# Kernel optimization log

Measured on AMD Instinct MI355X. Metric: run time of the kernel, lower is better.

Reference implementation:

```python
import jax, jax.numpy as jnp
import numpy as np

B, L = 32, 2048
AA_VOCAB, AA_EMB = 26, 5
C = 256                 # num_channels
S = 8                   # prot_section_size
GO_VOCAB, GO = 30000, 256
K = 15                  # conv kernel size


def setup_inputs() -> dict:
    key = jax.random.key(0)
    ks = jax.random.split(key, 10)
    inp = {
        "input_seq": jax.random.randint(ks[0], (B, L), 0, AA_VOCAB),
        "input_go_term": jax.random.randint(ks[1], (B,), 0, GO_VOCAB),
        "aa_emb": jax.random.normal(ks[2], (AA_VOCAB, AA_EMB), jnp.float32),
        "conv1_w": jax.random.normal(ks[3], (2 * C, AA_EMB, K), jnp.float32) * 0.05,
        "conv1_b": jnp.zeros((2 * C,), jnp.float32),
        "conv2_w": jax.random.normal(ks[4], (C, 2 * C, K), jnp.float32) * 0.02,
        "conv2_b": jnp.zeros((C,), jnp.float32),
        "go_table": jax.random.normal(ks[5], (GO_VOCAB, GO), jnp.float32),
        "attn_w": jax.random.normal(ks[6], (GO, C * S), jnp.float32) * 0.02,
        "attn_b": jnp.zeros((GO,), jnp.float32),
    }
    return inp


def reference(input_seq, input_go_term, aa_emb, conv1_w, conv1_b,
              conv2_w, conv2_b, go_table, attn_w, attn_b):
    # --- ProteinEncoder (dropout = identity at inference) ---
    x = aa_emb[input_seq]                      # [B, L, 5]
    x = jnp.transpose(x, (0, 2, 1))            # [B, 5, L]
    dn = ('NCH', 'OIH', 'NCH')
    x = jax.lax.conv_general_dilated(x, conv1_w, (1,), 'VALID', dimension_numbers=dn)
    x = jax.nn.relu(x + conv1_b[None, :, None])   # [B, 2C, L-14]
    x = jax.lax.conv_general_dilated(x, conv2_w, (1,), 'VALID', dimension_numbers=dn)
    x = jax.nn.relu(x + conv2_b[None, :, None])   # [B, C, P], P = L-28

    # --- section the protein (same row-major view as torch .view) ---
    b, c, P = x.shape
    n = P // S
    rem = P % S
    head = rem // 2
    tail = P - (rem - head)
    enc = x[:, :, head:tail].reshape(b, c * S, n)   # [B, C*S, N]

    # --- Attn('general'): score_i = go . (W @ section_i + bias), softmax over i ---
    go = go_table[input_go_term]                     # [B, G]
    proj = jnp.einsum('bpn,gp->bgn', enc, attn_w) + attn_b[:, None]  # [B, G, N]
    energies = jnp.einsum('bg,bgn->bn', go, proj)    # [B, N]
    attn = jax.nn.softmax(energies, axis=-1)         # [B, N]

    # --- context: [B,1,N] bmm [B,N,C*S] -> [B, C*S] ---
    ctx = jnp.einsum('bn,bpn->bp', attn, enc)
    return ctx
```

## Files before the change

### kernel.cpp

```cpp
#include <hip/hip_runtime.h>

#define B_ 32
#define L_ 2048
#define C1 512
#define C2 256
#define KW 15
#define P1 2034
#define NJ 2016
#define NSEC 252
#define GOD 256

typedef _Float16 f16;
typedef __attribute__((ext_vector_type(4))) _Float16 f16x4;
typedef __attribute__((ext_vector_type(8))) _Float16 f16x8;
typedef __attribute__((ext_vector_type(4))) float f32x4;

#define WS_Y1T   0ull
#define WS_W2R   66650112ull
#define WS_W1R   70582272ull
#define WS_E     70688768ull
#define WS_V     103718912ull
#define WS_EN    103981056ull
#define WS_ATTN  104013312ull

__device__ __forceinline__ void gl16(const f16* g, f16* l) {
    __builtin_amdgcn_global_load_lds((const __attribute__((address_space(1))) char*)(g),
                                     (__attribute__((address_space(3))) char*)(l), 16, 0, 0);
}

__global__ void k_w2r(const float* __restrict__ w2, f16* __restrict__ w2r) {
    const int n = C2 * C1 * KW;
    for (int idx = blockIdx.x * blockDim.x + threadIdx.x; idx < n; idx += gridDim.x * blockDim.x) {
        int o = idx / (C1 * KW);
        int rem = idx - o * (C1 * KW);
        int c = rem / KW;
        int k = rem - c * KW;
        w2r[((size_t)k * C2 + o) * C1 + c] = (f16)w2[idx];
    }
}

__global__ void k_w1r(const float* __restrict__ w1, f16* __restrict__ w1r) {
    const int n = C1 * 104;
    for (int idx = blockIdx.x * blockDim.x + threadIdx.x; idx < n; idx += gridDim.x * blockDim.x) {
        int o = idx / 104;
        int col = idx - o * 104;
        int e = col >> 4, k = col & 15;
        float val = (e < 5 && k < 15) ? w1[o * 75 + e * 15 + k] : 0.f;
        w1r[idx] = (f16)val;
    }
}

__global__ __launch_bounds__(256) void k_conv1(const int* __restrict__ seq,
                                               const float* __restrict__ aa_emb,
                                               const f16* __restrict__ w1r,
                                               const float* __restrict__ b1,
                                               f16* __restrict__ y1t) {
    __shared__ f16 Aw[256 * 104];
    __shared__ f16 Bx[64 * 104];
    __shared__ float xs[5][80];
    const int b = blockIdx.z, o0 = blockIdx.y * 256, pos0 = blockIdx.x * 64;
    const int tid = threadIdx.x;
    const int wave = tid >> 6, lane = tid & 63;
    const int lm = lane & 15, lh = lane >> 4;

#pragma unroll
    for (int r = 0; r < 13; ++r) {
        int q = r * 4096 + wave * 1024 + lane * 16;
        gl16(w1r + o0 * 104 + (q >> 1), Aw + (q >> 1));
    }
    if (tid < 79) {
        int l = pos0 + tid;
        if (l < L_) {
            int a = seq[b * L_ + l];
#pragma unroll
            for (int e = 0; e < 5; ++e) xs[e][tid] = aa_emb[a * 5 + e];
        } else {
#pragma unroll
            for (int e = 0; e < 5; ++e) xs[e][tid] = 0.f;
        }
    }
    __syncthreads();
    for (int idx = tid; idx < 64 * 104; idx += 256) {
        int j = idx / 104, col = idx - j * 104;
        int e = col >> 4, k = col & 15;
        Bx[idx] = (e < 5 && k < 15) ? (f16)xs[e][j + k] : (f16)0.f;
    }
    __syncthreads();

    f32x4 acc[4][4];
#pragma unroll
    for (int mf = 0; mf < 4; ++mf)
#pragma unroll
        for (int nf = 0; nf < 4; ++nf) acc[mf][nf] = (f32x4){0.f, 0.f, 0.f, 0.f};

    const char* Ab = (const char*)Aw + (wave * 64 + lm) * 208 + lh * 16;
    const char* Bb = (const char*)Bx + lm * 208 + lh * 16;
#pragma unroll
    for (int ks = 0; ks < 3; ++ks) {
        f16x8 av[4], bv[4];
#pragma unroll
        for (int mf = 0; mf < 4; ++mf) av[mf] = *(const f16x8*)(Ab + mf * 16 * 208 + ks * 64);
#pragma unroll
        for (int nf = 0; nf < 4; ++nf) bv[nf] = *(const f16x8*)(Bb + nf * 16 * 208 + ks * 64);
#pragma unroll
        for (int mf = 0; mf < 4; ++mf)
#pragma unroll
            for (int nf = 0; nf < 4; ++nf)
                acc[mf][nf] = __builtin_amdgcn_mfma_f32_16x16x32_f16(av[mf], bv[nf], acc[mf][nf], 0, 0, 0);
    }

#pragma unroll
    for (int nf = 0; nf < 4; ++nf) {
        int pos = pos0 + nf * 16 + lm;
        if (pos >= P1) continue;
#pragma unroll
        for (int mf = 0; mf < 4; ++mf) {
            int ob = wave * 64 + mf * 16 + lh * 4;
            f16x4 st;
#pragma unroll
            for (int r = 0; r < 4; ++r)
                st[r] = (f16)fmaxf(acc[mf][nf][r] + b1[o0 + ob + r], 0.f);
            *(f16x4*)(y1t + ((size_t)b * P1 + pos) * C1 + o0 + ob) = st;
        }
    }
}

__global__ __launch_bounds__(256, 2) void k_conv2(const f16* __restrict__ y1t,
                                                  const f16* __restrict__ w2r,
                                                  const float* __restrict__ b2,
                                                  const float* __restrict__ v,
                                                  f16* __restrict__ E,
                                                  float* __restrict__ energies) {
    __shared__ f16 As[3 * 8192];
    __shared__ f16 Bs[10240];
    const int b = blockIdx.y;
    const int n0 = blockIdx.x << 7;
    const int tid = threadIdx.x;
    const int wave = tid >> 6, lane = tid & 63;
    const int lm = lane & 15, lh = lane >> 4;
    const int wm = wave >> 1, wn = wave & 1;
    const size_t ybase = (size_t)b * P1 + n0 + 2;

    f32x4 acc[8][4];
#pragma unroll
    for (int mf = 0; mf < 8; ++mf)
#pragma unroll
        for (int nf = 0; nf < 4; ++nf) acc[mf][nf] = (f32x4){0.f, 0.f, 0.f, 0.f};

#define STAGE_A(slot, cc2, k2, h2)                                                    \
    {                                                                                 \
        _Pragma("unroll")                                                             \
        for (int rr = 0; rr < 4; ++rr) {                                              \
            int q = rr * 4096 + tid * 16;                                             \
            int row = q >> 6;                                                         \
            int sw = ((q >> 4) & 3) ^ ((row >> 1) & 3);                               \
            const f16* g = w2r + (size_t)(k2) * 131072 + row * C1 + (cc2) * 64 + (h2) * 32 + sw * 8; \
            gl16(g, As + (slot) * 8192 + (q >> 1));                                   \
        }                                                                             \
    }
#define STAGE_B(cc2)                                                                  \
    {                                                                                 \
        _Pragma("unroll")                                                             \
        for (int rr = 0; rr < 5; ++rr) {                                              \
            int q = rr * 4096 + tid * 16;                                             \
            int row = q >> 7;                                                         \
            int sw = ((q >> 4) & 7) ^ (row & 7);                                      \
            const f16* g = y1t + (ybase + row) * C1 + (cc2) * 64 + sw * 8;            \
            gl16(g, Bs + (q >> 1));                                                   \
        }                                                                             \
    }

    STAGE_B(0);
    STAGE_A(0, 0, 0, 0);
    STAGE_A(1, 0, 0, 1);
    asm volatile("s_waitcnt vmcnt(4)" ::: "memory");
    __builtin_amdgcn_s_barrier();

    const int swA = (lh ^ ((lm >> 1) & 3)) << 4;
    int sl = 0;

#pragma unroll 1
    for (int cc = 0; cc < 8; ++cc) {
#pragma unroll 1
        for (int k = 0; k < KW; ++k) {
#pragma unroll
            for (int h = 0; h < 2; ++h) {
                int k2 = k + 1, cc2 = cc;
                if (k2 == 15) { k2 = 0; cc2 = cc + 1; }
                const bool have2 = (cc2 < 8);
                const bool bnd = (k == 0 && h == 0 && cc > 0);
                const int s2 = (sl >= 1) ? sl - 1 : 2;

                if (bnd) {
                    STAGE_B(cc);
                    STAGE_A(s2, cc2, k2, h);
                    asm volatile("s_waitcnt vmcnt(4)" ::: "memory");
                    __builtin_amdgcn_s_barrier();
                }

                const char* Ab = (const char*)As + sl * 16384;
                f16x8 bv[4], av[8];
#pragma unroll
                for (int nf = 0; nf < 4; ++nf) {
                    int brow = wn * 64 + nf * 16 + lm + k;
                    bv[nf] = *(const f16x8*)((const char*)Bs + brow * 128 + ((((h << 2) | lh) ^ (brow & 7)) << 4));
                }
#pragma unroll
                for (int i = 0; i < 8; ++i)
                    av[i] = *(const f16x8*)(Ab + (wm * 128 + i * 16 + lm) * 64 + swA);
                if (!bnd && have2) STAGE_A(s2, cc2, k2, h);

                __builtin_amdgcn_s_barrier();
                __builtin_amdgcn_s_setprio(1);
#pragma unroll
                for (int i = 0; i < 8; ++i)
#pragma unroll
                    for (int nf = 0; nf < 4; ++nf)
                        acc[i][nf] = __builtin_amdgcn_mfma_f32_16x16x32_f16(av[i], bv[nf], acc[i][nf], 0, 0, 0);
                __builtin_amdgcn_s_setprio(0);
                if (have2) { asm volatile("s_waitcnt vmcnt(4)" ::: "memory"); }
                else       { asm volatile("s_waitcnt vmcnt(0)" ::: "memory"); }
                __builtin_amdgcn_s_barrier();

                sl = (sl == 2) ? 0 : sl + 1;
            }
        }
    }

    const float* vb = v + b * 2048;
#pragma unroll
    for (int nf = 0; nf < 4; ++nf) {
        const int j = n0 + wn * 64 + nf * 16 + lm;
        if (j >= NJ) continue;
        const int jq = j / NSEC;
        const int jm = j - jq * NSEC;
        float esum = 0.f;
#pragma unroll
        for (int mf = 0; mf < 8; ++mf) {
            const int ob = wm * 128 + mf * 16 + lh * 4;
#pragma unroll
            for (int r = 0; r < 4; ++r) {
                float val = fmaxf(acc[mf][nf][r] + b2[ob + r], 0.f);
                E[((size_t)b * C2 + ob + r) * NJ + j] = (f16)val;
                esum = fmaf(val, vb[(ob + r) * 8 + jq], esum);
            }
        }
        atomicAdd(&energies[b * NSEC + jm], esum);
    }
#undef STAGE_A
#undef STAGE_B
}

__global__ void k_v(const int* __restrict__ goidx, const float* __restrict__ go_table,
                    const float* __restrict__ attn_w, float* __restrict__ v) {
    const int b = blockIdx.y;
    const int p = blockIdx.x * 256 + threadIdx.x;
    const float* go = go_table + (size_t)goidx[b] * GOD;
    float acc = 0.f;
    for (int g = 0; g < GOD; ++g) acc = fmaf(go[g], attn_w[g * 2048 + p], acc);
    v[b * 2048 + p] = acc;
}

__global__ void k_softmax(const float* __restrict__ energies, float* __restrict__ attn) {
    const int b = blockIdx.x;
    const int n = threadIdx.x;
    __shared__ float red[256];
    float ev = 0.f;
    float e = -1e30f;
    if (n < NSEC) { ev = energies[b * NSEC + n]; e = ev; }
    red[n] = e;
    __syncthreads();
    for (int s = 128; s > 0; s >>= 1) {
        if (n < s) red[n] = fmaxf(red[n], red[n + s]);
        __syncthreads();
    }
    float m = red[0];
    __syncthreads();
    float ex = (n < NSEC) ? __expf(ev - m) : 0.f;
    red[n] = ex;
    __syncthreads();
    for (int s = 128; s > 0; s >>= 1) {
        if (n < s) red[n] += red[n + s];
        __syncthreads();
    }
    float inv = 1.f / red[0];
    if (n < NSEC) attn[b * NSEC + n] = ex * inv;
}

__global__ void k_ctx(const f16* __restrict__ E, const float* __restrict__ attn,
                      float* __restrict__ out) {
    const int b = blockIdx.y;
    const int wave = threadIdx.x >> 6, lane = threadIdx.x & 63;
    const int c = blockIdx.x * 4 + wave;
    float a0 = 0.f, a1 = 0.f, a2 = 0.f, a3 = 0.f;
    if (lane < 63) {
        const float* ap = attn + b * NSEC + lane * 4;
        a0 = ap[0]; a1 = ap[1]; a2 = ap[2]; a3 = ap[3];
    }
    const f16* Er = E + ((size_t)b * C2 + c) * NJ;
#pragma unroll
    for (int r = 0; r < 8; ++r) {
        float s = 0.f;
        if (lane < 63) {
            f16x4 e = *(const f16x4*)(Er + r * NSEC + lane * 4);
            s = (float)e[0] * a0 + (float)e[1] * a1 + (float)e[2] * a2 + (float)e[3] * a3;
        }
#pragma unroll
        for (int off = 32; off > 0; off >>= 1) s += __shfl_down(s, off);
        if (lane == 0) out[b * 2048 + c * 8 + r] = s;
    }
}

extern "C" void kernel_launch(void* const* d_in, const int* in_sizes, int n_in,
                              void* d_out, int out_size, void* d_ws, size_t ws_size,
                              hipStream_t stream) {
    const int*   seq      = (const int*)d_in[0];
    const int*   goidx    = (const int*)d_in[1];
    const float* aa_emb   = (const float*)d_in[2];
    const float* w1       = (const float*)d_in[3];
    const float* b1       = (const float*)d_in[4];
    const float* w2       = (const float*)d_in[5];
    const float* b2       = (const float*)d_in[6];
    const float* go_table = (const float*)d_in[7];
    const float* attn_w   = (const float*)d_in[8];
    float* out = (float*)d_out;

    char* ws = (char*)d_ws;
    f16*   y1t      = (f16*)(ws + WS_Y1T);
    f16*   w2r      = (f16*)(ws + WS_W2R);
    f16*   w1r      = (f16*)(ws + WS_W1R);
    f16*   E        = (f16*)(ws + WS_E);
    float* v        = (float*)(ws + WS_V);
    float* energies = (float*)(ws + WS_EN);
    float* attn     = (float*)(ws + WS_ATTN);

    hipMemsetAsync(energies, 0, B_ * NSEC * sizeof(float), stream);
    hipLaunchKernelGGL(k_w2r,     dim3(512),         dim3(256), 0, stream, w2, w2r);
    hipLaunchKernelGGL(k_w1r,     dim3(64),          dim3(256), 0, stream, w1, w1r);
    hipLaunchKernelGGL(k_conv1,   dim3(32, 2, B_),   dim3(256), 0, stream, seq, aa_emb, w1r, b1, y1t);
    hipLaunchKernelGGL(k_v,       dim3(8, B_),       dim3(256), 0, stream, goidx, go_table, attn_w, v);
    hipLaunchKernelGGL(k_conv2,   dim3(16, B_),      dim3(256), 0, stream, y1t, w2r, b2, v, E, energies);
    hipLaunchKernelGGL(k_softmax, dim3(B_),          dim3(256), 0, stream, energies, attn);
    hipLaunchKernelGGL(k_ctx,     dim3(64, B_),      dim3(256), 0, stream, E, attn, out);
}
```

Before: 284.4 us.

## Split conv2 output channels across blocks and batch GO projection over all sequences

The conv2 GEMM kernel now uses 128-thread blocks, each covering half of the output channels (grid gains an M dimension). Its A-tile pipeline drops from triple to double buffering with waits that fully drain outstanding loads. This doubles the block count to improve occupancy and CU coverage, but each block reloads the full activation tile, and the full drains reduce load/compute overlap. Separately, k_v loads all 32 GO vectors into shared memory so each attn_w element is read once and reused across the batch instead of once per batch.

```diff
diff --git a/kernel.cpp b/kernel.cpp
--- a/kernel.cpp
+++ b/kernel.cpp
@@ -125,20 +125,20 @@
     }
 }
 
-__global__ __launch_bounds__(256, 2) void k_conv2(const f16* __restrict__ y1t,
+__global__ __launch_bounds__(128, 2) void k_conv2(const f16* __restrict__ y1t,
                                                   const f16* __restrict__ w2r,
                                                   const float* __restrict__ b2,
                                                   const float* __restrict__ v,
                                                   f16* __restrict__ E,
                                                   float* __restrict__ energies) {
-    __shared__ f16 As[3 * 8192];
-    __shared__ f16 Bs[10240];
-    const int b = blockIdx.y;
+    __shared__ f16 As[2 * 4096];
+    __shared__ f16 Bs[9216];
+    const int b = blockIdx.z;
+    const int m0 = blockIdx.y;
     const int n0 = blockIdx.x << 7;
     const int tid = threadIdx.x;
-    const int wave = tid >> 6, lane = tid & 63;
+    const int wn = tid >> 6, lane = tid & 63;
     const int lm = lane & 15, lh = lane >> 4;
-    const int wm = wave >> 1, wn = wave & 1;
     const size_t ybase = (size_t)b * P1 + n0 + 2;
 
     f32x4 acc[8][4];
@@ -151,18 +151,18 @@
     {                                                                                 \
         _Pragma("unroll")                                                             \
         for (int rr = 0; rr < 4; ++rr) {                                              \
-            int q = rr * 4096 + tid * 16;                                             \
+            int q = rr * 2048 + tid * 16;                                             \
             int row = q >> 6;                                                         \
             int sw = ((q >> 4) & 3) ^ ((row >> 1) & 3);                               \
-            const f16* g = w2r + (size_t)(k2) * 131072 + row * C1 + (cc2) * 64 + (h2) * 32 + sw * 8; \
-            gl16(g, As + (slot) * 8192 + (q >> 1));                                   \
+            const f16* g = w2r + (size_t)(k2) * 131072 + (m0 * 128 + row) * C1 + (cc2) * 64 + (h2) * 32 + sw * 8; \
+            gl16(g, As + (slot) * 4096 + (q >> 1));                                   \
         }                                                                             \
     }
 #define STAGE_B(cc2)                                                                  \
     {                                                                                 \
         _Pragma("unroll")                                                             \
-        for (int rr = 0; rr < 5; ++rr) {                                              \
-            int q = rr * 4096 + tid * 16;                                             \
+        for (int rr = 0; rr < 9; ++rr) {                                              \
+            int q = rr * 2048 + tid * 16;                                             \
             int row = q >> 7;                                                         \
             int sw = ((q >> 4) & 7) ^ (row & 7);                                      \
             const f16* g = y1t + (ybase + row) * C1 + (cc2) * 64 + sw * 8;            \
@@ -172,45 +172,34 @@
 
     STAGE_B(0);
     STAGE_A(0, 0, 0, 0);
-    STAGE_A(1, 0, 0, 1);
-    asm volatile("s_waitcnt vmcnt(4)" ::: "memory");
+    asm volatile("s_waitcnt vmcnt(0)" ::: "memory");
     __builtin_amdgcn_s_barrier();
 
     const int swA = (lh ^ ((lm >> 1) & 3)) << 4;
-    int sl = 0;
+    int cur = 0;
 
 #pragma unroll 1
     for (int cc = 0; cc < 8; ++cc) {
 #pragma unroll 1
         for (int k = 0; k < KW; ++k) {
-#pragma unroll
-            for (int h = 0; h < 2; ++h) {
-                int k2 = k + 1, cc2 = cc;
-                if (k2 == 15) { k2 = 0; cc2 = cc + 1; }
-                const bool have2 = (cc2 < 8);
-                const bool bnd = (k == 0 && h == 0 && cc > 0);
-                const int s2 = (sl >= 1) ? sl - 1 : 2;
-
+            {
+                const bool bnd = (k == 0 && cc > 0);
+                if (bnd) STAGE_B(cc);
+                STAGE_A(cur ^ 1, cc, k, 1);
                 if (bnd) {
-                    STAGE_B(cc);
-                    STAGE_A(s2, cc2, k2, h);
-                    asm volatile("s_waitcnt vmcnt(4)" ::: "memory");
+                    asm volatile("s_waitcnt vmcnt(0)" ::: "memory");
                     __builtin_amdgcn_s_barrier();
                 }
-
-                const char* Ab = (const char*)As + sl * 16384;
+                const char* Ab = (const char*)As + cur * 8192;
                 f16x8 bv[4], av[8];
 #pragma unroll
                 for (int nf = 0; nf < 4; ++nf) {
                     int brow = wn * 64 + nf * 16 + lm + k;
-                    bv[nf] = *(const f16x8*)((const char*)Bs + brow * 128 + ((((h << 2) | lh) ^ (brow & 7)) << 4));
+                    bv[nf] = *(const f16x8*)((const char*)Bs + brow * 128 + ((lh ^ (brow & 7)) << 4));
                 }
 #pragma unroll
                 for (int i = 0; i < 8; ++i)
-                    av[i] = *(const f16x8*)(Ab + (wm * 128 + i * 16 + lm) * 64 + swA);
-                if (!bnd && have2) STAGE_A(s2, cc2, k2, h);
-
-                __builtin_amdgcn_s_barrier();
+                    av[i] = *(const f16x8*)(Ab + (i * 16 + lm) * 64 + swA);
                 __builtin_amdgcn_s_setprio(1);
 #pragma unroll
                 for (int i = 0; i < 8; ++i)
@@ -218,11 +207,34 @@
                     for (int nf = 0; nf < 4; ++nf)
                         acc[i][nf] = __builtin_amdgcn_mfma_f32_16x16x32_f16(av[i], bv[nf], acc[i][nf], 0, 0, 0);
                 __builtin_amdgcn_s_setprio(0);
-                if (have2) { asm volatile("s_waitcnt vmcnt(4)" ::: "memory"); }
-                else       { asm volatile("s_waitcnt vmcnt(0)" ::: "memory"); }
+                asm volatile("s_waitcnt vmcnt(0)" ::: "memory");
                 __builtin_amdgcn_s_barrier();
-
-                sl = (sl == 2) ? 0 : sl + 1;
+                cur ^= 1;
+            }
+            {
+                int k2 = (k == 14) ? 0 : k + 1;
+                int cc2 = (k == 14) ? cc + 1 : cc;
+                if (cc2 < 8) STAGE_A(cur ^ 1, cc2, k2, 0);
+                const char* Ab = (const char*)As + cur * 8192;
+                f16x8 bv[4], av[8];
+#pragma unroll
+                for (int nf = 0; nf < 4; ++nf) {
+                    int brow = wn * 64 + nf * 16 + lm + k;
+                    bv[nf] = *(const f16x8*)((const char*)Bs + brow * 128 + (((4 | lh) ^ (brow & 7)) << 4));
+                }
+#pragma unroll
+                for (int i = 0; i < 8; ++i)
+                    av[i] = *(const f16x8*)(Ab + (i * 16 + lm) * 64 + swA);
+                __builtin_amdgcn_s_setprio(1);
+#pragma unroll
+                for (int i = 0; i < 8; ++i)
+#pragma unroll
+                    for (int nf = 0; nf < 4; ++nf)
+                        acc[i][nf] = __builtin_amdgcn_mfma_f32_16x16x32_f16(av[i], bv[nf], acc[i][nf], 0, 0, 0);
+                __builtin_amdgcn_s_setprio(0);
+                asm volatile("s_waitcnt vmcnt(0)" ::: "memory");
+                __builtin_amdgcn_s_barrier();
+                cur ^= 1;
             }
         }
     }
@@ -237,7 +249,7 @@
         float esum = 0.f;
 #pragma unroll
         for (int mf = 0; mf < 8; ++mf) {
-            const int ob = wm * 128 + mf * 16 + lh * 4;
+            const int ob = m0 * 128 + mf * 16 + lh * 4;
 #pragma unroll
             for (int r = 0; r < 4; ++r) {
                 float val = fmaxf(acc[mf][nf][r] + b2[ob + r], 0.f);
@@ -251,14 +263,28 @@
 #undef STAGE_B
 }
 
-__global__ void k_v(const int* __restrict__ goidx, const float* __restrict__ go_table,
-                    const float* __restrict__ attn_w, float* __restrict__ v) {
-    const int b = blockIdx.y;
-    const int p = blockIdx.x * 256 + threadIdx.x;
-    const float* go = go_table + (size_t)goidx[b] * GOD;
-    float acc = 0.f;
-    for (int g = 0; g < GOD; ++g) acc = fmaf(go[g], attn_w[g * 2048 + p], acc);
-    v[b * 2048 + p] = acc;
+__global__ __launch_bounds__(256) void k_v(const int* __restrict__ goidx,
+                                           const float* __restrict__ go_table,
+                                           const float* __restrict__ attn_w,
+                                           float* __restrict__ v) {
+    __shared__ float go_s[32][GOD];
+    const int tid = threadIdx.x;
+    const int p = blockIdx.x * 256 + tid;
+    for (int idx = tid; idx < 32 * GOD; idx += 256) {
+        int bb = idx >> 8, g = idx & (GOD - 1);
+        go_s[bb][g] = go_table[(size_t)goidx[bb] * GOD + g];
+    }
+    __syncthreads();
+    float acc[32];
+#pragma unroll
+    for (int bb = 0; bb < 32; ++bb) acc[bb] = 0.f;
+    for (int g = 0; g < GOD; ++g) {
+        float w = attn_w[(size_t)g * 2048 + p];
+#pragma unroll
+        for (int bb = 0; bb < 32; ++bb) acc[bb] = fmaf(go_s[bb][g], w, acc[bb]);
+    }
+#pragma unroll
+    for (int bb = 0; bb < 32; ++bb) v[bb * 2048 + p] = acc[bb];
 }
 
 __global__ void k_softmax(const float* __restrict__ energies, float* __restrict__ attn) {
@@ -338,8 +364,8 @@
     hipLaunchKernelGGL(k_w2r,     dim3(512),         dim3(256), 0, stream, w2, w2r);
     hipLaunchKernelGGL(k_w1r,     dim3(64),          dim3(256), 0, stream, w1, w1r);
     hipLaunchKernelGGL(k_conv1,   dim3(32, 2, B_),   dim3(256), 0, stream, seq, aa_emb, w1r, b1, y1t);
-    hipLaunchKernelGGL(k_v,       dim3(8, B_),       dim3(256), 0, stream, goidx, go_table, attn_w, v);
-    hipLaunchKernelGGL(k_conv2,   dim3(16, B_),      dim3(256), 0, stream, y1t, w2r, b2, v, E, energies);
+    hipLaunchKernelGGL(k_v,       dim3(8),           dim3(256), 0, stream, goidx, go_table, attn_w, v);
+    hipLaunchKernelGGL(k_conv2,   dim3(16, 2, B_),   dim3(128), 0, stream, y1t, w2r, b2, v, E, energies);
     hipLaunchKernelGGL(k_softmax, dim3(B_),          dim3(256), 0, stream, energies, attn);
     hipLaunchKernelGGL(k_ctx,     dim3(64, B_),      dim3(256), 0, stream, E, attn, out);
 }
```

Result: slower. 360.5 us (+26.8%).

## Load conv2 weight fragments directly from global into registers, drop LDS staging

Applied to the files above, without the earlier changes.

The conv2 weights are re-laid out as [k][c/32][o][32] so each lane can read its MFMA A-fragment straight from global memory into registers, double-buffered across the two channel halves. The three-slot LDS ring for weights and most per-step barriers go away; LDS now holds only the input tile, which is restaged once per channel chunk. This removes LDS traffic and sync overhead, but weight reads now rely on L2/cache hits, and the input restage at each chunk boundary is no longer overlapped with compute.

```diff
diff --git a/kernel.cpp b/kernel.cpp
--- a/kernel.cpp
+++ b/kernel.cpp
@@ -35,7 +35,7 @@
         int rem = idx - o * (C1 * KW);
         int c = rem / KW;
         int k = rem - c * KW;
-        w2r[((size_t)k * C2 + o) * C1 + c] = (f16)w2[idx];
+        w2r[((k * 16 + (c >> 5)) * 256 + o) * 32 + (c & 31)] = (f16)w2[idx];
     }
 }
 
@@ -131,7 +131,6 @@
                                                   const float* __restrict__ v,
                                                   f16* __restrict__ E,
                                                   float* __restrict__ energies) {
-    __shared__ f16 As[3 * 8192];
     __shared__ f16 Bs[10240];
     const int b = blockIdx.y;
     const int n0 = blockIdx.x << 7;
@@ -147,17 +146,6 @@
 #pragma unroll
         for (int nf = 0; nf < 4; ++nf) acc[mf][nf] = (f32x4){0.f, 0.f, 0.f, 0.f};
 
-#define STAGE_A(slot, cc2, k2, h2)                                                    \
-    {                                                                                 \
-        _Pragma("unroll")                                                             \
-        for (int rr = 0; rr < 4; ++rr) {                                              \
-            int q = rr * 4096 + tid * 16;                                             \
-            int row = q >> 6;                                                         \
-            int sw = ((q >> 4) & 3) ^ ((row >> 1) & 3);                               \
-            const f16* g = w2r + (size_t)(k2) * 131072 + row * C1 + (cc2) * 64 + (h2) * 32 + sw * 8; \
-            gl16(g, As + (slot) * 8192 + (q >> 1));                                   \
-        }                                                                             \
-    }
 #define STAGE_B(cc2)                                                                  \
     {                                                                                 \
         _Pragma("unroll")                                                             \
@@ -170,60 +158,64 @@
         }                                                                             \
     }
 
+    const f16* gA = w2r + (wm * 128 + lm) * 32 + lh * 8;
+#define LOAD_A(dst, c5idx, kk)                                                        \
+    {                                                                                 \
+        const f16* ga = gA + ((kk) * 16 + (c5idx)) * 8192;                            \
+        _Pragma("unroll")                                                             \
+        for (int i = 0; i < 8; ++i) dst[i] = *(const f16x8*)(ga + i * 512);           \
+    }
+
+    f16x8 avA[8], avB[8];
+
     STAGE_B(0);
-    STAGE_A(0, 0, 0, 0);
-    STAGE_A(1, 0, 0, 1);
-    asm volatile("s_waitcnt vmcnt(4)" ::: "memory");
+    LOAD_A(avA, 0, 0);
+    asm volatile("s_waitcnt vmcnt(0)" ::: "memory");
     __builtin_amdgcn_s_barrier();
-
-    const int swA = (lh ^ ((lm >> 1) & 3)) << 4;
-    int sl = 0;
 
 #pragma unroll 1
     for (int cc = 0; cc < 8; ++cc) {
 #pragma unroll 1
         for (int k = 0; k < KW; ++k) {
-#pragma unroll
-            for (int h = 0; h < 2; ++h) {
-                int k2 = k + 1, cc2 = cc;
-                if (k2 == 15) { k2 = 0; cc2 = cc + 1; }
-                const bool have2 = (cc2 < 8);
-                const bool bnd = (k == 0 && h == 0 && cc > 0);
-                const int s2 = (sl >= 1) ? sl - 1 : 2;
-
-                if (bnd) {
-                    STAGE_B(cc);
-                    STAGE_A(s2, cc2, k2, h);
-                    asm volatile("s_waitcnt vmcnt(4)" ::: "memory");
-                    __builtin_amdgcn_s_barrier();
-                }
-
-                const char* Ab = (const char*)As + sl * 16384;
-                f16x8 bv[4], av[8];
+            LOAD_A(avB, cc * 2 + 1, k);
+            {
+                f16x8 bv[4];
 #pragma unroll
                 for (int nf = 0; nf < 4; ++nf) {
                     int brow = wn * 64 + nf * 16 + lm + k;
-                    bv[nf] = *(const f16x8*)((const char*)Bs + brow * 128 + ((((h << 2) | lh) ^ (brow & 7)) << 4));
+                    bv[nf] = *(const f16x8*)((const char*)Bs + brow * 128 + ((lh ^ (brow & 7)) << 4));
                 }
+                __builtin_amdgcn_s_setprio(1);
 #pragma unroll
                 for (int i = 0; i < 8; ++i)
-                    av[i] = *(const f16x8*)(Ab + (wm * 128 + i * 16 + lm) * 64 + swA);
-                if (!bnd && have2) STAGE_A(s2, cc2, k2, h);
-
-                __builtin_amdgcn_s_barrier();
+#pragma unroll
+                    for (int nf = 0; nf < 4; ++nf)
+                        acc[i][nf] = __builtin_amdgcn_mfma_f32_16x16x32_f16(avA[i], bv[nf], acc[i][nf], 0, 0, 0);
+                __builtin_amdgcn_s_setprio(0);
+            }
+            if (k < 14)      LOAD_A(avA, cc * 2, k + 1)
+            else if (cc < 7) LOAD_A(avA, cc * 2 + 2, 0)
+            {
+                f16x8 bv[4];
+#pragma unroll
+                for (int nf = 0; nf < 4; ++nf) {
+                    int brow = wn * 64 + nf * 16 + lm + k;
+                    bv[nf] = *(const f16x8*)((const char*)Bs + brow * 128 + (((4 | lh) ^ (brow & 7)) << 4));
+                }
                 __builtin_amdgcn_s_setprio(1);
 #pragma unroll
                 for (int i = 0; i < 8; ++i)
 #pragma unroll
                     for (int nf = 0; nf < 4; ++nf)
-                        acc[i][nf] = __builtin_amdgcn_mfma_f32_16x16x32_f16(av[i], bv[nf], acc[i][nf], 0, 0, 0);
+                        acc[i][nf] = __builtin_amdgcn_mfma_f32_16x16x32_f16(avB[i], bv[nf], acc[i][nf], 0, 0, 0);
                 __builtin_amdgcn_s_setprio(0);
-                if (have2) { asm volatile("s_waitcnt vmcnt(4)" ::: "memory"); }
-                else       { asm volatile("s_waitcnt vmcnt(0)" ::: "memory"); }
-                __builtin_amdgcn_s_barrier();
-
-                sl = (sl == 2) ? 0 : sl + 1;
             }
+        }
+        if (cc < 7) {
+            __builtin_amdgcn_s_barrier();
+            STAGE_B(cc + 1);
+            asm volatile("s_waitcnt vmcnt(0)" ::: "memory");
+            __builtin_amdgcn_s_barrier();
         }
     }
 
@@ -247,8 +239,8 @@
         }
         atomicAdd(&energies[b * NSEC + jm], esum);
     }
-#undef STAGE_A
 #undef STAGE_B
+#undef LOAD_A
 }
 
 __global__ void k_v(const int* __restrict__ goidx, const float* __restrict__ go_table,
```

Result: slower. 324.3 us (+14.0%).
